# Performance work log

Hardware: AMD Instinct MI355X
Metric: run time of the kernel (lower is better)

## Reference

```python
import jax, jax.numpy as jnp
import numpy as np

N_USERS = 100000
N_ENTITIES = 50000
D = 64
NNZ = 2000000


def setup_inputs() -> dict:
    key = jax.random.key(0)
    k1, k2, k3, k4, k5 = jax.random.split(key, 5)
    return {
        "user_emb": jax.random.normal(k1, (N_USERS, D), dtype=jnp.float32),
        "entity_emb": jax.random.normal(k2, (N_ENTITIES, D), dtype=jnp.float32),
        "rows": jax.random.randint(k3, (NNZ,), 0, N_USERS, dtype=jnp.int32),
        "cols": jax.random.randint(k4, (NNZ,), 0, N_ENTITIES, dtype=jnp.int32),
        "vals": jax.random.uniform(k5, (NNZ,), dtype=jnp.float32),
    }


def reference(user_emb, entity_emb, rows, cols, vals):
    # interact_mat is COO sparse [n_users, n_entities] with (rows, cols, vals).
    # entity_agg = interact_mat.T @ user_emb : scatter-add user rows into entity bins
    entity_agg = jax.ops.segment_sum(
        vals[:, None] * user_emb[rows], cols, num_segments=entity_emb.shape[0]
    )
    # user_agg = interact_mat @ entity_emb : scatter-add entity rows into user bins
    user_agg = jax.ops.segment_sum(
        vals[:, None] * entity_emb[cols], rows, num_segments=user_emb.shape[0]
    )
    return entity_agg, user_agg
```

## Files before the change

kernel.cpp:

```cpp
#include <hip/hip_runtime.h>

#define DIM 64
#define PBITS 6
#define PART_BUCKETS 64
#define NPART_MAX 2368
#define EPT 8
#define EPB (EPT * 1024)
#define CAP 2944
#define RECK ((CAP + 255) / 256)

__global__ void coo_scatter_kernel(const float* __restrict__ user_emb,
                                   const float* __restrict__ entity_emb,
                                   const int* __restrict__ rows,
                                   const int* __restrict__ cols,
                                   const float* __restrict__ vals,
                                   float* __restrict__ entity_agg,
                                   float* __restrict__ user_agg,
                                   int nnz) {
    long long tid = (long long)blockIdx.x * blockDim.x + threadIdx.x;
    long long total = (long long)nnz * DIM;
    if (tid >= total) return;
    int edge = (int)(tid >> 6);
    int d = (int)(tid & 63);
    int r = rows[edge];
    int c = cols[edge];
    float v = vals[edge];
    atomicAdd(&entity_agg[c * DIM + d], v * user_emb[r * DIM + d]);
    atomicAdd(&user_agg[r * DIM + d], v * entity_emb[c * DIM + d]);
}


__global__ __launch_bounds__(1024) void pass0_hist(const int* __restrict__ rows,
                                                   const int* __restrict__ cols,
                                                   int* __restrict__ pcnt,
                                                   int ne, int nnz, int npart) {
    __shared__ int h[NPART_MAX];
    for (int t = threadIdx.x; t < npart; t += 1024) h[t] = 0;
    __syncthreads();
    for (int i = blockIdx.x * blockDim.x + threadIdx.x; i < nnz;
         i += gridDim.x * blockDim.x) {
        int c = cols[i];
        int r = rows[i];
        atomicAdd(&h[c >> PBITS], 1);
        atomicAdd(&h[(ne + r) >> PBITS], 1);
    }
    __syncthreads();
    for (int t = threadIdx.x; t < npart; t += 1024)
        if (h[t]) atomicAdd(&pcnt[t], h[t]);
}

__global__ __launch_bounds__(256) void scan_parts(const int* __restrict__ pcnt,
                                                  int* __restrict__ poffs,
                                                  int* __restrict__ pcursor,
                                                  int* __restrict__ ovfcnt,
                                                  int npart) {
    __shared__ int sh[256];
    int t = threadIdx.x;
    int local[10];
    int s = 0;
#pragma unroll
    for (int j = 0; j < 10; ++j) {
        int idx = t * 10 + j;
        local[j] = (idx < npart) ? pcnt[idx] : 0;
        s += local[j];
    }
    sh[t] = s;
    for (int off = 1; off < 256; off <<= 1) {
        __syncthreads();
        int tmp = (t >= off) ? sh[t - off] : 0;
        __syncthreads();
        sh[t] += tmp;
    }
    __syncthreads();
    int run = sh[t] - s;
#pragma unroll
    for (int j = 0; j < 10; ++j) {
        int idx = t * 10 + j;
        if (idx < npart) {
            poffs[idx] = run;
            pcursor[idx] = run;
            run += local[j];
        }
    }
    if (t == 255) poffs[npart] = sh[255];
    if (t == 0) *ovfcnt = 0;
}

__global__ __launch_bounds__(1024) void pass1_part(const int* __restrict__ rows,
                                                   const int* __restrict__ cols,
                                                   const float* __restrict__ vals,
                                                   int* __restrict__ pcursor,
                                                   uint2* __restrict__ payload,
                                                   int ne, int nnz, int npart) {
    __shared__ int hist[NPART_MAX];
    __shared__ int cur[NPART_MAX];
    __shared__ int gbase[NPART_MAX];
    for (int t = threadIdx.x; t < npart; t += 1024) { hist[t] = 0; cur[t] = 0; }
    __syncthreads();

    int base = blockIdx.x * EPB;
#pragma unroll
    for (int k = 0; k < EPT; ++k) {
        int i = base + threadIdx.x + k * 1024;
        if (i < nnz) {
            atomicAdd(&hist[cols[i] >> PBITS], 1);
            atomicAdd(&hist[(ne + rows[i]) >> PBITS], 1);
        }
    }
    __syncthreads();
    for (int p = threadIdx.x; p < npart; p += 1024) {
        int c_ = hist[p];
        if (c_) gbase[p] = atomicAdd(&pcursor[p], c_);
    }
    __syncthreads();
#pragma unroll
    for (int k = 0; k < EPT; ++k) {
        int i = base + threadIdx.x + k * 1024;
        if (i < nnz) {
            int r = rows[i];
            int c = cols[i];
            unsigned vb = __float_as_uint(vals[i]);
            int b2 = ne + r;
            int p1 = c >> PBITS;
            int p2 = b2 >> PBITS;
            int rank1 = atomicAdd(&cur[p1], 1);
            payload[(size_t)gbase[p1] + rank1] =
                make_uint2(((unsigned)(c & (PART_BUCKETS - 1)) << 18) | (unsigned)r, vb);
            int rank2 = atomicAdd(&cur[p2], 1);
            payload[(size_t)gbase[p2] + rank2] =
                make_uint2(((unsigned)(b2 & (PART_BUCKETS - 1)) << 18) | (1u << 17) | (unsigned)c, vb);
        }
    }
}

__global__ __launch_bounds__(256) void sort_agg(const float* __restrict__ user_emb,
                                                const float* __restrict__ entity_emb,
                                                const uint2* __restrict__ payload,
                                                const int* __restrict__ poffs,
                                                int* __restrict__ ovfcnt,
                                                int* __restrict__ ovflist,
                                                float* __restrict__ out,
                                                int nb) {
    __shared__ uint2 srec[CAP];
    __shared__ int h[PART_BUCKETS], sc[PART_BUCKETS], cu[PART_BUCKETS];
    int p = blockIdx.x;
    int beg = poffs[p];
    int n = poffs[p + 1] - beg;
    int t = threadIdx.x;
    if (t < PART_BUCKETS) h[t] = 0;
    __syncthreads();

    if (n > CAP) {
        if (t == 0) {
            int o = atomicAdd(ovfcnt, 1);
            ovflist[o] = p;
        }
        int b0 = p << PBITS;
        for (int e = t; e < PART_BUCKETS * DIM; e += 256) {
            int b = b0 + (e >> 6);
            if (b < nb) out[(size_t)b * DIM + (e & 63)] = 0.f;
        }
        return;
    }

    uint2 rec[RECK];
#pragma unroll
    for (int k = 0; k < RECK; ++k) {
        int idx = t + k * 256;
        if (idx < n) {
            rec[k] = payload[(size_t)beg + idx];
            atomicAdd(&h[(rec[k].x >> 18) & (PART_BUCKETS - 1)], 1);
        }
    }
    __syncthreads();
    if (t == 0) {
        int run = 0;
#pragma unroll
        for (int j = 0; j < PART_BUCKETS; ++j) { sc[j] = run; cu[j] = run; run += h[j]; }
    }
    __syncthreads();
#pragma unroll
    for (int k = 0; k < RECK; ++k) {
        int idx = t + k * 256;
        if (idx < n) {
            int b = (rec[k].x >> 18) & (PART_BUCKETS - 1);
            int rank = atomicAdd(&cu[b], 1);
            srec[rank] = rec[k];
        }
    }
    __syncthreads();

    int wid = t >> 6;
    int lane = t & 63;
    int grp = lane >> 4;
    int sub = lane & 15;

    for (int bi = 0; bi < 16; ++bi) {
        int lb = wid * 16 + bi;
        int bucket = (p << PBITS) + lb;
        int rb = sc[lb];
        int cnt = h[lb];

        float ax0 = 0.f, ay0 = 0.f, az0 = 0.f, aw0 = 0.f;
        float ax1 = 0.f, ay1 = 0.f, az1 = 0.f, aw1 = 0.f;
        float ax2 = 0.f, ay2 = 0.f, az2 = 0.f, aw2 = 0.f;
        float ax3 = 0.f, ay3 = 0.f, az3 = 0.f, aw3 = 0.f;

        int i = 0;
        for (; i + 16 <= cnt; i += 16) {
            uint2 r0 = srec[rb + i + grp];
            uint2 r1 = srec[rb + i + 4 + grp];
            uint2 r2 = srec[rb + i + 8 + grp];
            uint2 r3 = srec[rb + i + 12 + grp];
            const float* __restrict__ t0 = (r0.x & (1u << 17)) ? entity_emb : user_emb;
            const float* __restrict__ t1 = (r1.x & (1u << 17)) ? entity_emb : user_emb;
            const float* __restrict__ t2 = (r2.x & (1u << 17)) ? entity_emb : user_emb;
            const float* __restrict__ t3 = (r3.x & (1u << 17)) ? entity_emb : user_emb;
            const float4 e0 = *(const float4*)(t0 + (size_t)(r0.x & 0x1FFFFu) * DIM + sub * 4);
            const float4 e1 = *(const float4*)(t1 + (size_t)(r1.x & 0x1FFFFu) * DIM + sub * 4);
            const float4 e2 = *(const float4*)(t2 + (size_t)(r2.x & 0x1FFFFu) * DIM + sub * 4);
            const float4 e3 = *(const float4*)(t3 + (size_t)(r3.x & 0x1FFFFu) * DIM + sub * 4);
            float v0 = __uint_as_float(r0.y);
            float v1 = __uint_as_float(r1.y);
            float v2 = __uint_as_float(r2.y);
            float v3 = __uint_as_float(r3.y);
            ax0 += v0 * e0.x; ay0 += v0 * e0.y; az0 += v0 * e0.z; aw0 += v0 * e0.w;
            ax1 += v1 * e1.x; ay1 += v1 * e1.y; az1 += v1 * e1.z; aw1 += v1 * e1.w;
            ax2 += v2 * e2.x; ay2 += v2 * e2.y; az2 += v2 * e2.z; aw2 += v2 * e2.w;
            ax3 += v3 * e3.x; ay3 += v3 * e3.y; az3 += v3 * e3.z; aw3 += v3 * e3.w;
        }
        for (; i + 8 <= cnt; i += 8) {
            uint2 rA = srec[rb + i + grp];
            uint2 rB = srec[rb + i + 4 + grp];
            const float* __restrict__ tA = (rA.x & (1u << 17)) ? entity_emb : user_emb;
            const float* __restrict__ tB = (rB.x & (1u << 17)) ? entity_emb : user_emb;
            const float4 eA = *(const float4*)(tA + (size_t)(rA.x & 0x1FFFFu) * DIM + sub * 4);
            const float4 eB = *(const float4*)(tB + (size_t)(rB.x & 0x1FFFFu) * DIM + sub * 4);
            float vA = __uint_as_float(rA.y);
            float vB = __uint_as_float(rB.y);
            ax0 += vA * eA.x; ay0 += vA * eA.y; az0 += vA * eA.z; aw0 += vA * eA.w;
            ax1 += vB * eB.x; ay1 += vB * eB.y; az1 += vB * eB.z; aw1 += vB * eB.w;
        }
        for (; i < cnt; i += 4) {
            int j = i + grp;
            bool valid = j < cnt;
            uint2 r = srec[rb + (valid ? j : cnt - 1)];
            const float* __restrict__ tb = (r.x & (1u << 17)) ? entity_emb : user_emb;
            const float4 e = *(const float4*)(tb + (size_t)(r.x & 0x1FFFFu) * DIM + sub * 4);
            float v = valid ? __uint_as_float(r.y) : 0.f;
            ax0 += v * e.x; ay0 += v * e.y; az0 += v * e.z; aw0 += v * e.w;
        }

        ax0 += ax1 + ax2 + ax3; ay0 += ay1 + ay2 + ay3;
        az0 += az1 + az2 + az3; aw0 += aw1 + aw2 + aw3;
        ax0 += __shfl_xor(ax0, 16, 64); ay0 += __shfl_xor(ay0, 16, 64);
        az0 += __shfl_xor(az0, 16, 64); aw0 += __shfl_xor(aw0, 16, 64);
        ax0 += __shfl_xor(ax0, 32, 64); ay0 += __shfl_xor(ay0, 32, 64);
        az0 += __shfl_xor(az0, 32, 64); aw0 += __shfl_xor(aw0, 32, 64);

        if (grp == 0 && bucket < nb) {
            float4 res = make_float4(ax0, ay0, az0, aw0);
            *(float4*)(out + (size_t)bucket * DIM + sub * 4) = res;
        }
    }
}

__global__ void pass3_ovf(const uint2* __restrict__ payload,
                          const int* __restrict__ poffs,
                          const int* __restrict__ ovfcnt,
                          const int* __restrict__ ovflist,
                          const float* __restrict__ user_emb,
                          const float* __restrict__ entity_emb,
                          float* __restrict__ out) {
    int no = *ovfcnt;
    for (int o = 0; o < no; ++o) {
        int p = ovflist[o];
        int beg = poffs[p];
        int n = poffs[p + 1] - beg;
        for (int j = blockIdx.x * blockDim.x + threadIdx.x; j < n * 16;
             j += gridDim.x * blockDim.x) {
            uint2 rec = payload[(size_t)beg + (j >> 4)];
            int d4 = (j & 15) * 4;
            const float* tab = (rec.x & (1u << 17)) ? entity_emb : user_emb;
            float v = __uint_as_float(rec.y);
            int bucket = (p << PBITS) | (int)((rec.x >> 18) & (PART_BUCKETS - 1));
            const float* src = tab + (size_t)(rec.x & 0x1FFFFu) * DIM + d4;
            float* dst = out + (size_t)bucket * DIM + d4;
            for (int d = 0; d < 4; ++d) atomicAdd(&dst[d], v * src[d]);
        }
    }
}

extern "C" void kernel_launch(void* const* d_in, const int* in_sizes, int n_in,
                              void* d_out, int out_size, void* d_ws, size_t ws_size,
                              hipStream_t stream) {
    const float* user_emb   = (const float*)d_in[0];
    const float* entity_emb = (const float*)d_in[1];
    const int*   rows       = (const int*)d_in[2];
    const int*   cols       = (const int*)d_in[3];
    const float* vals       = (const float*)d_in[4];
    int nnz = in_sizes[2];
    int nu  = in_sizes[0] / DIM;
    int ne  = in_sizes[1] / DIM;
    int nb  = ne + nu;
    int npart = (nb + PART_BUCKETS - 1) / PART_BUCKETS;

    float* out = (float*)d_out;

    size_t n_ints = (size_t)npart * 4 + 2;
    size_t pay_off_ints = (n_ints + 1) & ~(size_t)1;
    size_t need = pay_off_ints * 4 + (size_t)2 * nnz * 8;

    if (ws_size < need || npart > NPART_MAX || nu > 131072 || ne > 131072) {
        float* entity_agg = out;
        float* user_agg   = out + (size_t)ne * DIM;
        hipMemsetAsync(d_out, 0, (size_t)out_size * sizeof(float), stream);
        long long total = (long long)nnz * DIM;
        int block = 256;
        long long grid = (total + block - 1) / block;
        coo_scatter_kernel<<<(int)grid, block, 0, stream>>>(
            user_emb, entity_emb, rows, cols, vals, entity_agg, user_agg, nnz);
        return;
    }

    int*   pcnt    = (int*)d_ws;
    int*   poffs   = pcnt + npart;
    int*   pcursor = poffs + npart + 1;
    int*   ovfcnt  = pcursor + npart;
    int*   ovflist = ovfcnt + 1;
    uint2* payload = (uint2*)((int*)d_ws + pay_off_ints);

    hipMemsetAsync(pcnt, 0, (size_t)npart * sizeof(int), stream);

    pass0_hist<<<256, 1024, 0, stream>>>(rows, cols, pcnt, ne, nnz, npart);
    scan_parts<<<1, 256, 0, stream>>>(pcnt, poffs, pcursor, ovfcnt, npart);
    int g1 = (nnz + EPB - 1) / EPB;
    pass1_part<<<g1, 1024, 0, stream>>>(rows, cols, vals, pcursor, payload, ne, nnz, npart);
    sort_agg<<<npart, 256, 0, stream>>>(user_emb, entity_emb, payload, poffs,
                                        ovfcnt, ovflist, out, nb);
    pass3_ovf<<<64, 256, 0, stream>>>(payload, poffs, ovfcnt, ovflist,
                                      user_emb, entity_emb, out);
}
```

Baseline: 210.2 us.

## Replace histogram and scan passes with fixed-capacity partition slots

Drops the global histogram pass and the prefix-scan kernel. Each partition now gets a fixed-capacity slot in the payload buffer (larger for entity partitions, smaller for user partitions), and pass1 appends into it with atomic counters. Partitions that exceed their capacity are flagged and recomputed by a fallback kernel that rescans every edge and uses atomics. This saves one full read of rows and cols plus two launches, at the cost of a larger workspace and an expensive fallback whenever a slot overflows.

```diff
diff --git a/kernel.cpp b/kernel.cpp
--- a/kernel.cpp
+++ b/kernel.cpp
@@ -6,8 +6,9 @@
 #define NPART_MAX 2368
 #define EPT 8
 #define EPB (EPT * 1024)
-#define CAP 2944
-#define RECK ((CAP + 255) / 256)
+#define CAPE 2944
+#define CAPU 1664
+#define RECK ((CAPE + 255) / 256)
 
 __global__ void coo_scatter_kernel(const float* __restrict__ user_emb,
                                    const float* __restrict__ entity_emb,
@@ -30,68 +31,20 @@
 }
 
 
-__global__ __launch_bounds__(1024) void pass0_hist(const int* __restrict__ rows,
-                                                   const int* __restrict__ cols,
-                                                   int* __restrict__ pcnt,
-                                                   int ne, int nnz, int npart) {
-    __shared__ int h[NPART_MAX];
-    for (int t = threadIdx.x; t < npart; t += 1024) h[t] = 0;
-    __syncthreads();
-    for (int i = blockIdx.x * blockDim.x + threadIdx.x; i < nnz;
-         i += gridDim.x * blockDim.x) {
-        int c = cols[i];
-        int r = rows[i];
-        atomicAdd(&h[c >> PBITS], 1);
-        atomicAdd(&h[(ne + r) >> PBITS], 1);
-    }
-    __syncthreads();
-    for (int t = threadIdx.x; t < npart; t += 1024)
-        if (h[t]) atomicAdd(&pcnt[t], h[t]);
-}
-
-__global__ __launch_bounds__(256) void scan_parts(const int* __restrict__ pcnt,
-                                                  int* __restrict__ poffs,
-                                                  int* __restrict__ pcursor,
-                                                  int* __restrict__ ovfcnt,
-                                                  int npart) {
-    __shared__ int sh[256];
-    int t = threadIdx.x;
-    int local[10];
-    int s = 0;
-#pragma unroll
-    for (int j = 0; j < 10; ++j) {
-        int idx = t * 10 + j;
-        local[j] = (idx < npart) ? pcnt[idx] : 0;
-        s += local[j];
-    }
-    sh[t] = s;
-    for (int off = 1; off < 256; off <<= 1) {
-        __syncthreads();
-        int tmp = (t >= off) ? sh[t - off] : 0;
-        __syncthreads();
-        sh[t] += tmp;
-    }
-    __syncthreads();
-    int run = sh[t] - s;
-#pragma unroll
-    for (int j = 0; j < 10; ++j) {
-        int idx = t * 10 + j;
-        if (idx < npart) {
-            poffs[idx] = run;
-            pcursor[idx] = run;
-            run += local[j];
-        }
-    }
-    if (t == 255) poffs[npart] = sh[255];
-    if (t == 0) *ovfcnt = 0;
+__device__ __forceinline__ size_t slotbase(int p, int npeC) {
+    return (p < npeC) ? (size_t)p * CAPE
+                      : (size_t)npeC * CAPE + (size_t)(p - npeC) * CAPU;
+}
+__device__ __forceinline__ int slotcap(int p, int npeC) {
+    return (p < npeC) ? CAPE : CAPU;
 }
 
 __global__ __launch_bounds__(1024) void pass1_part(const int* __restrict__ rows,
                                                    const int* __restrict__ cols,
                                                    const float* __restrict__ vals,
-                                                   int* __restrict__ pcursor,
+                                                   int* __restrict__ cnt,
                                                    uint2* __restrict__ payload,
-                                                   int ne, int nnz, int npart) {
+                                                   int ne, int nnz, int npart, int npeC) {
     __shared__ int hist[NPART_MAX];
     __shared__ int cur[NPART_MAX];
     __shared__ int gbase[NPART_MAX];
@@ -110,7 +63,7 @@
     __syncthreads();
     for (int p = threadIdx.x; p < npart; p += 1024) {
         int c_ = hist[p];
-        if (c_) gbase[p] = atomicAdd(&pcursor[p], c_);
+        if (c_) gbase[p] = atomicAdd(&cnt[p], c_);
     }
     __syncthreads();
 #pragma unroll
@@ -123,12 +76,14 @@
             int b2 = ne + r;
             int p1 = c >> PBITS;
             int p2 = b2 >> PBITS;
-            int rank1 = atomicAdd(&cur[p1], 1);
-            payload[(size_t)gbase[p1] + rank1] =
-                make_uint2(((unsigned)(c & (PART_BUCKETS - 1)) << 18) | (unsigned)r, vb);
-            int rank2 = atomicAdd(&cur[p2], 1);
-            payload[(size_t)gbase[p2] + rank2] =
-                make_uint2(((unsigned)(b2 & (PART_BUCKETS - 1)) << 18) | (1u << 17) | (unsigned)c, vb);
+            int s1 = gbase[p1] + atomicAdd(&cur[p1], 1);
+            if (s1 < slotcap(p1, npeC))
+                payload[slotbase(p1, npeC) + s1] =
+                    make_uint2(((unsigned)(c & (PART_BUCKETS - 1)) << 18) | (unsigned)r, vb);
+            int s2 = gbase[p2] + atomicAdd(&cur[p2], 1);
+            if (s2 < slotcap(p2, npeC))
+                payload[slotbase(p2, npeC) + s2] =
+                    make_uint2(((unsigned)(b2 & (PART_BUCKETS - 1)) << 18) | (1u << 17) | (unsigned)c, vb);
         }
     }
 }
@@ -136,24 +91,25 @@
 __global__ __launch_bounds__(256) void sort_agg(const float* __restrict__ user_emb,
                                                 const float* __restrict__ entity_emb,
                                                 const uint2* __restrict__ payload,
-                                                const int* __restrict__ poffs,
+                                                const int* __restrict__ cnt,
                                                 int* __restrict__ ovfcnt,
-                                                int* __restrict__ ovflist,
+                                                unsigned char* __restrict__ ovfflag,
                                                 float* __restrict__ out,
-                                                int nb) {
-    __shared__ uint2 srec[CAP];
+                                                int nb, int npeC) {
+    __shared__ uint2 srec[CAPE];
     __shared__ int h[PART_BUCKETS], sc[PART_BUCKETS], cu[PART_BUCKETS];
     int p = blockIdx.x;
-    int beg = poffs[p];
-    int n = poffs[p + 1] - beg;
+    size_t beg = slotbase(p, npeC);
+    int cap = slotcap(p, npeC);
+    int n = cnt[p];
     int t = threadIdx.x;
     if (t < PART_BUCKETS) h[t] = 0;
     __syncthreads();
 
-    if (n > CAP) {
+    if (n > cap) {
         if (t == 0) {
-            int o = atomicAdd(ovfcnt, 1);
-            ovflist[o] = p;
+            atomicAdd(ovfcnt, 1);
+            ovfflag[p] = 1;
         }
         int b0 = p << PBITS;
         for (int e = t; e < PART_BUCKETS * DIM; e += 256) {
@@ -168,7 +124,7 @@
     for (int k = 0; k < RECK; ++k) {
         int idx = t + k * 256;
         if (idx < n) {
-            rec[k] = payload[(size_t)beg + idx];
+            rec[k] = payload[beg + idx];
             atomicAdd(&h[(rec[k].x >> 18) & (PART_BUCKETS - 1)], 1);
         }
     }
@@ -199,7 +155,7 @@
         int lb = wid * 16 + bi;
         int bucket = (p << PBITS) + lb;
         int rb = sc[lb];
-        int cnt = h[lb];
+        int cntb = h[lb];
 
         float ax0 = 0.f, ay0 = 0.f, az0 = 0.f, aw0 = 0.f;
         float ax1 = 0.f, ay1 = 0.f, az1 = 0.f, aw1 = 0.f;
@@ -207,7 +163,7 @@
         float ax3 = 0.f, ay3 = 0.f, az3 = 0.f, aw3 = 0.f;
 
         int i = 0;
-        for (; i + 16 <= cnt; i += 16) {
+        for (; i + 16 <= cntb; i += 16) {
             uint2 r0 = srec[rb + i + grp];
             uint2 r1 = srec[rb + i + 4 + grp];
             uint2 r2 = srec[rb + i + 8 + grp];
@@ -229,7 +185,7 @@
             ax2 += v2 * e2.x; ay2 += v2 * e2.y; az2 += v2 * e2.z; aw2 += v2 * e2.w;
             ax3 += v3 * e3.x; ay3 += v3 * e3.y; az3 += v3 * e3.z; aw3 += v3 * e3.w;
         }
-        for (; i + 8 <= cnt; i += 8) {
+        for (; i + 8 <= cntb; i += 8) {
             uint2 rA = srec[rb + i + grp];
             uint2 rB = srec[rb + i + 4 + grp];
             const float* __restrict__ tA = (rA.x & (1u << 17)) ? entity_emb : user_emb;
@@ -241,10 +197,10 @@
             ax0 += vA * eA.x; ay0 += vA * eA.y; az0 += vA * eA.z; aw0 += vA * eA.w;
             ax1 += vB * eB.x; ay1 += vB * eB.y; az1 += vB * eB.z; aw1 += vB * eB.w;
         }
-        for (; i < cnt; i += 4) {
+        for (; i < cntb; i += 4) {
             int j = i + grp;
-            bool valid = j < cnt;
-            uint2 r = srec[rb + (valid ? j : cnt - 1)];
+            bool valid = j < cntb;
+            uint2 r = srec[rb + (valid ? j : cntb - 1)];
             const float* __restrict__ tb = (r.x & (1u << 17)) ? entity_emb : user_emb;
             const float4 e = *(const float4*)(tb + (size_t)(r.x & 0x1FFFFu) * DIM + sub * 4);
             float v = valid ? __uint_as_float(r.y) : 0.f;
@@ -265,28 +221,30 @@
     }
 }
 
-__global__ void pass3_ovf(const uint2* __restrict__ payload,
-                          const int* __restrict__ poffs,
-                          const int* __restrict__ ovfcnt,
-                          const int* __restrict__ ovflist,
-                          const float* __restrict__ user_emb,
-                          const float* __restrict__ entity_emb,
-                          float* __restrict__ out) {
-    int no = *ovfcnt;
-    for (int o = 0; o < no; ++o) {
-        int p = ovflist[o];
-        int beg = poffs[p];
-        int n = poffs[p + 1] - beg;
-        for (int j = blockIdx.x * blockDim.x + threadIdx.x; j < n * 16;
-             j += gridDim.x * blockDim.x) {
-            uint2 rec = payload[(size_t)beg + (j >> 4)];
-            int d4 = (j & 15) * 4;
-            const float* tab = (rec.x & (1u << 17)) ? entity_emb : user_emb;
-            float v = __uint_as_float(rec.y);
-            int bucket = (p << PBITS) | (int)((rec.x >> 18) & (PART_BUCKETS - 1));
-            const float* src = tab + (size_t)(rec.x & 0x1FFFFu) * DIM + d4;
-            float* dst = out + (size_t)bucket * DIM + d4;
-            for (int d = 0; d < 4; ++d) atomicAdd(&dst[d], v * src[d]);
+__global__ void pass3_rescan(const int* __restrict__ rows,
+                             const int* __restrict__ cols,
+                             const float* __restrict__ vals,
+                             const float* __restrict__ user_emb,
+                             const float* __restrict__ entity_emb,
+                             const int* __restrict__ ovfcnt,
+                             const unsigned char* __restrict__ ovfflag,
+                             float* __restrict__ out, int ne, int nnz) {
+    if (*ovfcnt == 0) return;
+    for (int i = blockIdx.x * blockDim.x + threadIdx.x; i < nnz;
+         i += gridDim.x * blockDim.x) {
+        int c = cols[i];
+        int r = rows[i];
+        float v = vals[i];
+        if (ovfflag[c >> PBITS]) {
+            const float* src = user_emb + (size_t)r * DIM;
+            float* dst = out + (size_t)c * DIM;
+            for (int d = 0; d < DIM; ++d) atomicAdd(&dst[d], v * src[d]);
+        }
+        int b2 = ne + r;
+        if (ovfflag[b2 >> PBITS]) {
+            const float* src = entity_emb + (size_t)c * DIM;
+            float* dst = out + (size_t)b2 * DIM;
+            for (int d = 0; d < DIM; ++d) atomicAdd(&dst[d], v * src[d]);
         }
     }
 }
@@ -303,15 +261,20 @@
     int nu  = in_sizes[0] / DIM;
     int ne  = in_sizes[1] / DIM;
     int nb  = ne + nu;
-    int npart = (nb + PART_BUCKETS - 1) / PART_BUCKETS;
+    int npart = (nb + PART_BUCKETS - 1) >> PBITS;
+    int npeC  = (ne + PART_BUCKETS - 1) >> PBITS;
 
     float* out = (float*)d_out;
 
-    size_t n_ints = (size_t)npart * 4 + 2;
-    size_t pay_off_ints = (n_ints + 1) & ~(size_t)1;
-    size_t need = pay_off_ints * 4 + (size_t)2 * nnz * 8;
-
-    if (ws_size < need || npart > NPART_MAX || nu > 131072 || ne > 131072) {
+    size_t meta_bytes = (size_t)npart * 4 + 4 + (size_t)npart;
+    size_t pay_off = (meta_bytes + 15) & ~(size_t)15;
+    size_t nslots = (size_t)npeC * CAPE + (size_t)(npart - npeC) * CAPU;
+    size_t need = pay_off + nslots * 8;
+    long long avg_e = (long long)nnz * PART_BUCKETS / (ne > 0 ? ne : 1);
+    long long avg_u = (long long)nnz * PART_BUCKETS / (nu > 0 ? nu : 1);
+
+    if (ws_size < need || npart > NPART_MAX || nu > 131072 || ne > 131072 ||
+        avg_e > 2700 || avg_u > 1500) {
         float* entity_agg = out;
         float* user_agg   = out + (size_t)ne * DIM;
         hipMemsetAsync(d_out, 0, (size_t)out_size * sizeof(float), stream);
@@ -323,21 +286,17 @@
         return;
     }
 
-    int*   pcnt    = (int*)d_ws;
-    int*   poffs   = pcnt + npart;
-    int*   pcursor = poffs + npart + 1;
-    int*   ovfcnt  = pcursor + npart;
-    int*   ovflist = ovfcnt + 1;
-    uint2* payload = (uint2*)((int*)d_ws + pay_off_ints);
-
-    hipMemsetAsync(pcnt, 0, (size_t)npart * sizeof(int), stream);
-
-    pass0_hist<<<256, 1024, 0, stream>>>(rows, cols, pcnt, ne, nnz, npart);
-    scan_parts<<<1, 256, 0, stream>>>(pcnt, poffs, pcursor, ovfcnt, npart);
+    int*           cnt     = (int*)d_ws;
+    int*           ovfcnt  = cnt + npart;
+    unsigned char* ovfflag = (unsigned char*)(ovfcnt + 1);
+    uint2*         payload = (uint2*)((char*)d_ws + pay_off);
+
+    hipMemsetAsync(d_ws, 0, meta_bytes, stream);
+
     int g1 = (nnz + EPB - 1) / EPB;
-    pass1_part<<<g1, 1024, 0, stream>>>(rows, cols, vals, pcursor, payload, ne, nnz, npart);
-    sort_agg<<<npart, 256, 0, stream>>>(user_emb, entity_emb, payload, poffs,
-                                        ovfcnt, ovflist, out, nb);
-    pass3_ovf<<<64, 256, 0, stream>>>(payload, poffs, ovfcnt, ovflist,
-                                      user_emb, entity_emb, out);
-}
+    pass1_part<<<g1, 1024, 0, stream>>>(rows, cols, vals, cnt, payload, ne, nnz, npart, npeC);
+    sort_agg<<<npart, 256, 0, stream>>>(user_emb, entity_emb, payload, cnt,
+                                        ovfcnt, ovfflag, out, nb, npeC);
+    pass3_rescan<<<512, 256, 0, stream>>>(rows, cols, vals, user_emb, entity_emb,
+                                          ovfcnt, ovfflag, out, ne, nnz);
+}
```

Result: faster. 201.4 us (-4.1%).
